# Kernel optimization log

Measured on AMD Instinct MI355X. Metric: run time of the kernel, lower is better.

Reference implementation:

```python
import jax, jax.numpy as jnp
import numpy as np

B, S, D = 4, 4096, 1024

def setup_inputs() -> dict:
    key = jax.random.key(0)
    ks = jax.random.split(key, 11)
    scale = 1.0 / np.sqrt(D)
    def lin(k):
        return jax.random.normal(k, (D, D), dtype=jnp.float32) * scale
    return {
        "x": jax.random.normal(ks[0], (B, S, D), dtype=jnp.float32),
        "Wq": lin(ks[1]), "bq": jax.random.normal(ks[2], (D,), dtype=jnp.float32) * 0.02,
        "Wk": lin(ks[3]), "bk": jax.random.normal(ks[4], (D,), dtype=jnp.float32) * 0.02,
        "Wv": lin(ks[5]), "bv": jax.random.normal(ks[6], (D,), dtype=jnp.float32) * 0.02,
        "W1": lin(ks[7]), "b1": jax.random.normal(ks[8], (D,), dtype=jnp.float32) * 0.02,
        "W2": lin(ks[9]), "b2": jax.random.normal(ks[10], (D,), dtype=jnp.float32) * 0.02,
    }

def reference(x, Wq, bq, Wk, bk, Wv, bv, W1, b1, W2, b2):
    d = x.shape[-1]
    # Single-head self-attention with residual (faithful to source)
    q = x @ Wq + bq  # [B,S,D]
    k = x @ Wk + bk
    v = x @ Wv + bv
    scores = jnp.einsum('bsd,btd->bst', q, k) / jnp.sqrt(jnp.float32(d))  # [B,S,S]
    attn = jax.nn.softmax(scores, axis=-1)
    x = x + jnp.einsum('bst,btd->bsd', attn, v)
    # FeedForward: fc2(relu(fc1(x))), then doubled (x = x + x in source)
    h = jax.nn.relu(x @ W1 + b1)
    y = h @ W2 + b2
    return y + y
```

## Files before the change

### kernel.cpp

```cpp
#include <hip/hip_runtime.h>
#include <stdint.h>

typedef unsigned short u16;
typedef __bf16 bf16x8 __attribute__((ext_vector_type(8)));
typedef float f32x4 __attribute__((ext_vector_type(4)));
typedef unsigned short u16x8 __attribute__((ext_vector_type(8)));
typedef unsigned short u16x4 __attribute__((ext_vector_type(4)));

__device__ __forceinline__ float b2f(u16 b) {
    return __uint_as_float(((unsigned)b) << 16);
}
__device__ __forceinline__ u16 f2b(float f) {
    unsigned u = __float_as_uint(f);
    unsigned r = (u + 0x7fffu + ((u >> 16) & 1u)) >> 16;
    return (u16)r;
}

#define GLDS16(g, l) __builtin_amdgcn_global_load_lds(                        \
    (const __attribute__((address_space(1))) void*)(g),                       \
    (__attribute__((address_space(3))) void*)(l), 16, 0, 0)

template<int HAS_BIAS, int RELU, int HAS_RES, int OUT_MODE>
__device__ __forceinline__ void gemm9_body(
    const u16* __restrict__ A, const u16* __restrict__ Bt,
    const float* __restrict__ bias, const float* __restrict__ res,
    void* __restrict__ Cout, int N, int K,
    long sA, long sB, long sC, long sR, float scale)
{
    __shared__ u16 smem[65536];

    const long nwg = (long)gridDim.x * gridDim.y * gridDim.z;
    long gid = ((long)blockIdx.z * gridDim.y + blockIdx.y) * gridDim.x + blockIdx.x;
    long logical = (nwg % 8 == 0) ? (gid & 7) * (nwg >> 3) + (gid >> 3) : gid;
    const int bx = (int)(logical % gridDim.x);
    long tmp = logical / gridDim.x;
    const int by = (int)(tmp % gridDim.y);
    const int bz = (int)(tmp / gridDim.y);

    A  += (long)bz * sA;
    Bt += (long)bz * sB;

    const int tid  = threadIdx.x;
    const int lane = tid & 63, wid = tid >> 6;
    const int wm   = wid >> 2, wn = wid & 3;
    const int lr   = lane & 15, lk = lane >> 4;
    const long m0  = (long)by * 256;
    const long n0  = (long)bx * 256;
    const int  NT  = K >> 6;

    const u16* gA0 = A  + (m0 + (tid >> 2)) * (long)K + (tid & 3) * 8;
    const u16* gB0 = Bt + (n0 + (tid >> 2)) * (long)K + (tid & 3) * 8;
    const u16* gA1 = gA0 + 128L * K;
    const u16* gB1 = gB0 + 128L * K;
    const int wdst = (tid & ~63) * 8;

#define STA(bufn, kk, kof) do {                                               \
    GLDS16(gA0 + (kof) + (kk) * 32, &smem[(bufn)*16384 + (kk)*8192 + wdst]);  \
    GLDS16(gA1 + (kof) + (kk) * 32, &smem[(bufn)*16384 + (kk)*8192 + wdst + 4096]); } while (0)
#define STB(bufn, kk, kof) do {                                               \
    GLDS16(gB0 + (kof) + (kk) * 32, &smem[32768 + (bufn)*16384 + (kk)*8192 + wdst]); \
    GLDS16(gB1 + (kof) + (kk) * 32, &smem[32768 + (bufn)*16384 + (kk)*8192 + wdst + 4096]); } while (0)

    const int raOff = (wm * 128 + lr) * 32 + lk * 8;
    const int rbOff = (wn * 64  + lr) * 32 + lk * 8;

#define DSA(dst, BUF, kk, ih) do { _Pragma("unroll")                          \
    for (int i = 0; i < 4; ++i)                                               \
        dst[i] = *(const bf16x8*)&smem[(BUF)*16384 + (kk)*8192 + raOff + ((ih)*4 + i)*512]; } while (0)
#define DSB(dst, BUF, kk) do { _Pragma("unroll")                              \
    for (int j = 0; j < 4; ++j)                                               \
        dst[j] = *(const bf16x8*)&smem[32768 + (BUF)*16384 + (kk)*8192 + rbOff + j*512]; } while (0)

#define LGK(n) do { asm volatile("s_waitcnt lgkmcnt(" #n ")" ::: "memory");   \
                    __builtin_amdgcn_sched_barrier(0); } while (0)
#define CKPT(n) do { asm volatile("s_waitcnt vmcnt(" #n ")" ::: "memory");    \
    __builtin_amdgcn_s_barrier(); __builtin_amdgcn_sched_barrier(0); } while (0)

#define MFM(IH, A_, B_) do { __builtin_amdgcn_s_setprio(1); _Pragma("unroll") \
    for (int i = 0; i < 4; ++i) _Pragma("unroll")                             \
        for (int j = 0; j < 4; ++j)                                           \
            acc[(IH)*4 + i][j] = __builtin_amdgcn_mfma_f32_16x16x32_bf16(     \
                A_[i], B_[j], acc[(IH)*4 + i][j], 0, 0, 0);                   \
    __builtin_amdgcn_s_setprio(0); } while (0)

#define TILE_MAIN(BUF, kof) do {                                              \
    DSA(aY, BUF, 0, 1);                 STA((BUF)^1, 0, kof);                 \
    LGK(4);  MFM(0, aX, bX);                                                  \
    CKPT(2);                                                                  \
    DSA(aX, BUF, 1, 0);  DSB(bY, BUF, 1);  STB((BUF)^1, 0, kof);              \
    LGK(8);  MFM(1, aY, bX);                                                  \
    DSA(aY, BUF, 1, 1);                 STA((BUF)^1, 1, kof);                 \
    LGK(4);  MFM(0, aX, bY);                                                  \
    CKPT(2);                                                                  \
    DSA(aX, (BUF)^1, 0, 0);  DSB(bX, (BUF)^1, 0);  STB((BUF)^1, 1, kof);      \
    LGK(8);  MFM(1, aY, bY);                                                  \
} while (0)

#define TILE_LAST(BUF) do {                                                   \
    DSA(aY, BUF, 0, 1);                                                       \
    LGK(4);  MFM(0, aX, bX);                                                  \
    CKPT(0);                                                                  \
    DSA(aX, BUF, 1, 0);  DSB(bY, BUF, 1);                                     \
    LGK(8);  MFM(1, aY, bX);                                                  \
    DSA(aY, BUF, 1, 1);                                                       \
    LGK(4);  MFM(0, aX, bY);                                                  \
    LGK(0);  MFM(1, aY, bY);                                                  \
} while (0)

    f32x4 acc[8][4];
    #pragma unroll
    for (int i = 0; i < 8; ++i)
        #pragma unroll
        for (int j = 0; j < 4; ++j)
            #pragma unroll
            for (int r = 0; r < 4; ++r) acc[i][j][r] = 0.0f;

    bf16x8 aX[4], aY[4], bX[4], bY[4];

    STA(0, 0, 0); STB(0, 0, 0); STA(0, 1, 0); STB(0, 1, 0);
    CKPT(4);
    DSA(aX, 0, 0, 0); DSB(bX, 0, 0);

    #pragma unroll 1
    for (int t = 0; t + 2 < NT; t += 2) {
        TILE_MAIN(0, (long)(t + 1) * 64);
        TILE_MAIN(1, (long)(t + 2) * 64);
    }
    TILE_MAIN(0, (long)(NT - 1) * 64);
    TILE_LAST(1);

    const long crow0 = m0 + wm * 128;
    const long ccol0 = n0 + wn * 64;
    u16*   Cb = (u16*)Cout   + (long)bz * sC;
    float* Cf = (float*)Cout + (long)bz * sC;
    const float* resz = res + (long)bz * sR;
    #pragma unroll
    for (int i = 0; i < 8; ++i) {
        #pragma unroll
        for (int j = 0; j < 4; ++j) {
            const long col = ccol0 + j * 16 + lr;
            float bv_ = 0.0f;
            if (HAS_BIAS) bv_ = bias[col];
            if (OUT_MODE == 2) {
                const long row0 = crow0 + i * 16 + lk * 4;
                u16x4 pk;
                #pragma unroll
                for (int r = 0; r < 4; ++r) {
                    float v = acc[i][j][r] + bv_;
                    v *= scale;
                    pk[r] = f2b(v);
                }
                const long b_ = row0 >> 12, s_ = row0 & 4095;
                *(u16x4*)((u16*)Cout + (b_ << 22) + (col << 12) + s_) = pk;
            } else {
                #pragma unroll
                for (int r = 0; r < 4; ++r) {
                    const long row = crow0 + i * 16 + lk * 4 + r;
                    float v = acc[i][j][r];
                    if (HAS_BIAS) v += bv_;
                    v *= scale;
                    if (RELU) v = fmaxf(v, 0.0f);
                    if (HAS_RES) v += resz[row * (long)N + col];
                    if (OUT_MODE == 1) Cf[row * (long)N + col] = v;
                    else               Cb[row * (long)N + col] = f2b(v);
                }
            }
        }
    }
#undef STA
#undef STB
#undef DSA
#undef DSB
#undef LGK
#undef CKPT
#undef MFM
#undef TILE_MAIN
#undef TILE_LAST
}

__global__ __launch_bounds__(512, 2) void g9_proj(
    const u16* A, const u16* Bt, const float* bias, u16* C, int N, int K)
{ gemm9_body<1,0,0,0>(A, Bt, bias, nullptr, C, N, K, 0,0,0,0, 1.0f); }

__global__ __launch_bounds__(512, 2) void g9_vproj(
    const u16* A, const u16* Bt, const float* bias, u16* C, int N, int K)
{ gemm9_body<1,0,0,2>(A, Bt, bias, nullptr, C, N, K, 0,0,0,0, 1.0f); }

__global__ __launch_bounds__(512, 2) void g9_qkt(
    const u16* A, const u16* Bt, u16* C, int N, int K,
    long sA, long sB, long sC, float scale)
{ gemm9_body<0,0,0,0>(A, Bt, nullptr, nullptr, C, N, K, sA, sB, sC, 0, scale); }

__global__ __launch_bounds__(512, 2) void g9_pv(
    const u16* A, const u16* Bt, const float* res, u16* C, int N, int K,
    long sA, long sB, long sC, long sR)
{ gemm9_body<0,0,1,0>(A, Bt, nullptr, res, C, N, K, sA, sB, sC, sR, 1.0f); }

__global__ __launch_bounds__(512, 2) void g9_ffn1(
    const u16* A, const u16* Bt, const float* bias, u16* C, int N, int K)
{ gemm9_body<1,1,0,0>(A, Bt, bias, nullptr, C, N, K, 0,0,0,0, 1.0f); }

__global__ __launch_bounds__(512, 2) void g9_ffn2(
    const u16* A, const u16* Bt, const float* bias, float* C, int N, int K, float scale)
{ gemm9_body<1,0,0,1>(A, Bt, bias, nullptr, C, N, K, 0,0,0,0, scale); }

__global__ __launch_bounds__(256) void cvt_f32_bf16(
    const float* __restrict__ in, u16* __restrict__ out, long n)
{
    long i = ((long)blockIdx.x * 256 + threadIdx.x) * 4;
    if (i >= n) return;
    float4 f = *(const float4*)(in + i);
    u16x4 o;
    o[0] = f2b(f.x); o[1] = f2b(f.y); o[2] = f2b(f.z); o[3] = f2b(f.w);
    *(u16x4*)(out + i) = o;
}

__global__ __launch_bounds__(256) void transpose_to_bf16(
    const float* __restrict__ in, u16* __restrict__ out, int R, int C)
{
    __shared__ float tile[32][33];
    const int bx = blockIdx.x * 32;
    const int by = blockIdx.y * 32;
    const int tx = threadIdx.x, ty = threadIdx.y;
    #pragma unroll
    for (int i = 0; i < 32; i += 8)
        tile[ty + i][tx] = in[(long)(by + ty + i) * C + bx + tx];
    __syncthreads();
    #pragma unroll
    for (int i = 0; i < 32; i += 8)
        out[(long)(bx + ty + i) * R + by + tx] = f2b(tile[tx][ty + i]);
}

__global__ __launch_bounds__(256) void softmax_rows(u16* __restrict__ P, int n)
{
    const int t = threadIdx.x;
    const int lane = t & 63, w = t >> 6;
    u16* row = P + (long)blockIdx.x * n;
    u16x8 a = *(const u16x8*)(row + t * 16);
    u16x8 b = *(const u16x8*)(row + t * 16 + 8);
    float v[16];
    #pragma unroll
    for (int i = 0; i < 8; ++i) { v[i] = b2f(a[i]); v[8 + i] = b2f(b[i]); }

    float mx = v[0];
    #pragma unroll
    for (int i = 1; i < 16; ++i) mx = fmaxf(mx, v[i]);
    #pragma unroll
    for (int o = 32; o > 0; o >>= 1) mx = fmaxf(mx, __shfl_xor(mx, o));
    __shared__ float red[8];
    if (lane == 0) red[w] = mx;
    __syncthreads();
    mx = fmaxf(fmaxf(red[0], red[1]), fmaxf(red[2], red[3]));

    float s = 0.0f;
    #pragma unroll
    for (int i = 0; i < 16; ++i) { v[i] = __expf(v[i] - mx); s += v[i]; }
    #pragma unroll
    for (int o = 32; o > 0; o >>= 1) s += __shfl_xor(s, o);
    if (lane == 0) red[4 + w] = s;
    __syncthreads();
    s = red[4] + red[5] + red[6] + red[7];
    const float inv = 1.0f / s;

    #pragma unroll
    for (int i = 0; i < 8; ++i) { a[i] = f2b(v[i] * inv); b[i] = f2b(v[8 + i] * inv); }
    *(u16x8*)(row + t * 16)     = a;
    *(u16x8*)(row + t * 16 + 8) = b;
}

extern "C" void kernel_launch(void* const* d_in, const int* in_sizes, int n_in,
                              void* d_out, int out_size, void* d_ws, size_t ws_size,
                              hipStream_t stream)
{
    (void)in_sizes; (void)n_in; (void)out_size;
    const float* x  = (const float*)d_in[0];
    const float* Wq = (const float*)d_in[1];
    const float* bq = (const float*)d_in[2];
    const float* Wk = (const float*)d_in[3];
    const float* bk = (const float*)d_in[4];
    const float* Wv = (const float*)d_in[5];
    const float* bv = (const float*)d_in[6];
    const float* W1 = (const float*)d_in[7];
    const float* b1 = (const float*)d_in[8];
    const float* W2 = (const float*)d_in[9];
    const float* b2 = (const float*)d_in[10];
    float* out = (float*)d_out;

    const int  B = 4, S = 4096, D = 1024;
    const long SD  = (long)S * D;
    const long BSD = (long)B * SD;
    const long SS  = (long)S * S;

    int BC = 4;
    while (BC > 1 && (size_t)((long)BC * SS + 5L * D * D + 3L * BSD) * 2 > ws_size)
        BC >>= 1;

    u16* Pb = (u16*)d_ws;
    u16* xb = Pb;
    u16* Wt = Pb + (long)BC * SS;
    u16* Qb = Wt + 5L * D * D;
    u16* Kb = Qb + BSD;
    u16* Vt = Kb + BSD;

    cvt_f32_bf16<<<dim3((unsigned)(BSD / 4 / 256)), 256, 0, stream>>>(x, xb, BSD);

    dim3 tb(32, 8);
    transpose_to_bf16<<<dim3(D / 32, D / 32), tb, 0, stream>>>(Wq, Wt + 0L * D * D, D, D);
    transpose_to_bf16<<<dim3(D / 32, D / 32), tb, 0, stream>>>(Wk, Wt + 1L * D * D, D, D);
    transpose_to_bf16<<<dim3(D / 32, D / 32), tb, 0, stream>>>(Wv, Wt + 2L * D * D, D, D);
    transpose_to_bf16<<<dim3(D / 32, D / 32), tb, 0, stream>>>(W1, Wt + 3L * D * D, D, D);
    transpose_to_bf16<<<dim3(D / 32, D / 32), tb, 0, stream>>>(W2, Wt + 4L * D * D, D, D);

    const dim3 gproj(D / 256, (B * S) / 256);
    g9_proj <<<gproj, 512, 0, stream>>>(xb, Wt + 0L*D*D, bq, Qb, D, D);
    g9_proj <<<gproj, 512, 0, stream>>>(xb, Wt + 1L*D*D, bk, Kb, D, D);
    g9_vproj<<<gproj, 512, 0, stream>>>(xb, Wt + 2L*D*D, bv, Vt, D, D);

    for (int c = 0; c < B; c += BC) {
        g9_qkt<<<dim3(S/256, S/256, BC), 512, 0, stream>>>(
            Qb + (long)c * SD, Kb + (long)c * SD, Pb, S, D, SD, SD, SS, 0.03125f);
        softmax_rows<<<BC * S, 256, 0, stream>>>(Pb, S);
        g9_pv<<<dim3(D/256, S/256, BC), 512, 0, stream>>>(
            Pb, Vt + (long)c * SD, x + (long)c * SD, Kb + (long)c * SD,
            D, S, SS, SD, SD, SD);
    }

    g9_ffn1<<<gproj, 512, 0, stream>>>(Kb, Wt + 3L*D*D, b1, Qb, D, D);
    g9_ffn2<<<gproj, 512, 0, stream>>>(Qb, Wt + 4L*D*D, b2, out, D, D, 2.0f);
}
```

Measured before the change: 546.2 us.

## Restructure GEMM main loop into full k-slice phases with deeper prefetch

The GEMM inner schedule now loads all 8 A fragments and 4 B fragments per k-slice and issues 32 MFMAs per phase, replacing the four half-tile phases. Global-to-LDS prefetch runs one extra half-tile ahead, with three stages in flight at the prologue and a separate penultimate tile step. The aim is fewer barriers and waitcnt points per tile and more latency hiding for the LDS loads. In exchange, A-fragment register usage doubles, which may pressure the 2-waves-per-SIMD occupancy target, and LDS buffer reuse becomes tighter.

```diff
diff --git a/kernel.cpp b/kernel.cpp
--- a/kernel.cpp
+++ b/kernel.cpp
@@ -21,7 +21,7 @@
     (__attribute__((address_space(3))) void*)(l), 16, 0, 0)
 
 template<int HAS_BIAS, int RELU, int HAS_RES, int OUT_MODE>
-__device__ __forceinline__ void gemm9_body(
+__device__ __forceinline__ void gemm10_body(
     const u16* __restrict__ A, const u16* __restrict__ Bt,
     const float* __restrict__ bias, const float* __restrict__ res,
     void* __restrict__ Cout, int N, int K,
@@ -64,10 +64,10 @@
     const int raOff = (wm * 128 + lr) * 32 + lk * 8;
     const int rbOff = (wn * 64  + lr) * 32 + lk * 8;
 
-#define DSA(dst, BUF, kk, ih) do { _Pragma("unroll")                          \
-    for (int i = 0; i < 4; ++i)                                               \
-        dst[i] = *(const bf16x8*)&smem[(BUF)*16384 + (kk)*8192 + raOff + ((ih)*4 + i)*512]; } while (0)
-#define DSB(dst, BUF, kk) do { _Pragma("unroll")                              \
+#define DSA8(dst, BUF, kk) do { _Pragma("unroll")                             \
+    for (int i = 0; i < 8; ++i)                                               \
+        dst[i] = *(const bf16x8*)&smem[(BUF)*16384 + (kk)*8192 + raOff + i*512]; } while (0)
+#define DSB4(dst, BUF, kk) do { _Pragma("unroll")                             \
     for (int j = 0; j < 4; ++j)                                               \
         dst[j] = *(const bf16x8*)&smem[32768 + (BUF)*16384 + (kk)*8192 + rbOff + j*512]; } while (0)
 
@@ -76,35 +76,34 @@
 #define CKPT(n) do { asm volatile("s_waitcnt vmcnt(" #n ")" ::: "memory");    \
     __builtin_amdgcn_s_barrier(); __builtin_amdgcn_sched_barrier(0); } while (0)
 
-#define MFM(IH, A_, B_) do { __builtin_amdgcn_s_setprio(1); _Pragma("unroll") \
-    for (int i = 0; i < 4; ++i) _Pragma("unroll")                             \
+#define MFM32(A_, B_) do { __builtin_amdgcn_s_setprio(1); _Pragma("unroll")   \
+    for (int i = 0; i < 8; ++i) _Pragma("unroll")                             \
         for (int j = 0; j < 4; ++j)                                           \
-            acc[(IH)*4 + i][j] = __builtin_amdgcn_mfma_f32_16x16x32_bf16(     \
-                A_[i], B_[j], acc[(IH)*4 + i][j], 0, 0, 0);                   \
+            acc[i][j] = __builtin_amdgcn_mfma_f32_16x16x32_bf16(              \
+                A_[i], B_[j], acc[i][j], 0, 0, 0);                            \
     __builtin_amdgcn_s_setprio(0); } while (0)
 
-#define TILE_MAIN(BUF, kof) do {                                              \
-    DSA(aY, BUF, 0, 1);                 STA((BUF)^1, 0, kof);                 \
-    LGK(4);  MFM(0, aX, bX);                                                  \
-    CKPT(2);                                                                  \
-    DSA(aX, BUF, 1, 0);  DSB(bY, BUF, 1);  STB((BUF)^1, 0, kof);              \
-    LGK(8);  MFM(1, aY, bX);                                                  \
-    DSA(aY, BUF, 1, 1);                 STA((BUF)^1, 1, kof);                 \
-    LGK(4);  MFM(0, aX, bY);                                                  \
-    CKPT(2);                                                                  \
-    DSA(aX, (BUF)^1, 0, 0);  DSB(bX, (BUF)^1, 0);  STB((BUF)^1, 1, kof);      \
-    LGK(8);  MFM(1, aY, bY);                                                  \
+#define TILE_FULL(BUF, kof1, kof2) do {                                       \
+    DSA8(aY, BUF, 1);  DSB4(bY, BUF, 1);                                      \
+    STA((BUF)^1, 1, kof1);  STB((BUF)^1, 1, kof1);                            \
+    LGK(12);  MFM32(aX, bX);  CKPT(4);                                        \
+    DSA8(aX, (BUF)^1, 0);  DSB4(bX, (BUF)^1, 0);                              \
+    STA(BUF, 0, kof2);  STB(BUF, 0, kof2);                                    \
+    LGK(12);  MFM32(aY, bY);  CKPT(4);                                        \
 } while (0)
 
+#define TILE_PEN(BUF, kof1) do {                                              \
+    DSA8(aY, BUF, 1);  DSB4(bY, BUF, 1);                                      \
+    STA((BUF)^1, 1, kof1);  STB((BUF)^1, 1, kof1);                            \
+    LGK(12);  MFM32(aX, bX);  CKPT(4);                                        \
+    DSA8(aX, (BUF)^1, 0);  DSB4(bX, (BUF)^1, 0);                              \
+    LGK(12);  MFM32(aY, bY);  CKPT(0);                                        \
+} while (0)
+
 #define TILE_LAST(BUF) do {                                                   \
-    DSA(aY, BUF, 0, 1);                                                       \
-    LGK(4);  MFM(0, aX, bX);                                                  \
-    CKPT(0);                                                                  \
-    DSA(aX, BUF, 1, 0);  DSB(bY, BUF, 1);                                     \
-    LGK(8);  MFM(1, aY, bX);                                                  \
-    DSA(aY, BUF, 1, 1);                                                       \
-    LGK(4);  MFM(0, aX, bY);                                                  \
-    LGK(0);  MFM(1, aY, bY);                                                  \
+    DSA8(aY, BUF, 1);  DSB4(bY, BUF, 1);                                      \
+    LGK(12);  MFM32(aX, bX);                                                  \
+    LGK(0);   MFM32(aY, bY);                                                  \
 } while (0)
 
     f32x4 acc[8][4];
@@ -115,18 +114,21 @@
             #pragma unroll
             for (int r = 0; r < 4; ++r) acc[i][j][r] = 0.0f;
 
-    bf16x8 aX[4], aY[4], bX[4], bY[4];
-
-    STA(0, 0, 0); STB(0, 0, 0); STA(0, 1, 0); STB(0, 1, 0);
+    bf16x8 aX[8], aY[8], bX[4], bY[4];
+
+    STA(0, 0, 0); STB(0, 0, 0);
+    STA(0, 1, 0); STB(0, 1, 0);
+    STA(1, 0, 64); STB(1, 0, 64);
+    CKPT(8);
+    DSA8(aX, 0, 0); DSB4(bX, 0, 0);
     CKPT(4);
-    DSA(aX, 0, 0, 0); DSB(bX, 0, 0);
 
     #pragma unroll 1
-    for (int t = 0; t + 2 < NT; t += 2) {
-        TILE_MAIN(0, (long)(t + 1) * 64);
-        TILE_MAIN(1, (long)(t + 2) * 64);
+    for (int t = 0; t + 3 < NT; t += 2) {
+        TILE_FULL(0, (long)(t + 1) * 64, (long)(t + 2) * 64);
+        TILE_FULL(1, (long)(t + 2) * 64, (long)(t + 3) * 64);
     }
-    TILE_MAIN(0, (long)(NT - 1) * 64);
+    TILE_PEN(0, (long)(NT - 1) * 64);
     TILE_LAST(1);
 
     const long crow0 = m0 + wm * 128;
@@ -169,40 +171,41 @@
     }
 #undef STA
 #undef STB
-#undef DSA
-#undef DSB
+#undef DSA8
+#undef DSB4
 #undef LGK
 #undef CKPT
-#undef MFM
-#undef TILE_MAIN
+#undef MFM32
+#undef TILE_FULL
+#undef TILE_PEN
 #undef TILE_LAST
 }
 
-__global__ __launch_bounds__(512, 2) void g9_proj(
+__global__ __launch_bounds__(512, 2) void g10_proj(
     const u16* A, const u16* Bt, const float* bias, u16* C, int N, int K)
-{ gemm9_body<1,0,0,0>(A, Bt, bias, nullptr, C, N, K, 0,0,0,0, 1.0f); }
-
-__global__ __launch_bounds__(512, 2) void g9_vproj(
+{ gemm10_body<1,0,0,0>(A, Bt, bias, nullptr, C, N, K, 0,0,0,0, 1.0f); }
+
+__global__ __launch_bounds__(512, 2) void g10_vproj(
     const u16* A, const u16* Bt, const float* bias, u16* C, int N, int K)
-{ gemm9_body<1,0,0,2>(A, Bt, bias, nullptr, C, N, K, 0,0,0,0, 1.0f); }
-
-__global__ __launch_bounds__(512, 2) void g9_qkt(
+{ gemm10_body<1,0,0,2>(A, Bt, bias, nullptr, C, N, K, 0,0,0,0, 1.0f); }
+
+__global__ __launch_bounds__(512, 2) void g10_qkt(
     const u16* A, const u16* Bt, u16* C, int N, int K,
     long sA, long sB, long sC, float scale)
-{ gemm9_body<0,0,0,0>(A, Bt, nullptr, nullptr, C, N, K, sA, sB, sC, 0, scale); }
-
-__global__ __launch_bounds__(512, 2) void g9_pv(
+{ gemm10_body<0,0,0,0>(A, Bt, nullptr, nullptr, C, N, K, sA, sB, sC, 0, scale); }
+
+__global__ __launch_bounds__(512, 2) void g10_pv(
     const u16* A, const u16* Bt, const float* res, u16* C, int N, int K,
     long sA, long sB, long sC, long sR)
-{ gemm9_body<0,0,1,0>(A, Bt, nullptr, res, C, N, K, sA, sB, sC, sR, 1.0f); }
-
-__global__ __launch_bounds__(512, 2) void g9_ffn1(
+{ gemm10_body<0,0,1,0>(A, Bt, nullptr, res, C, N, K, sA, sB, sC, sR, 1.0f); }
+
+__global__ __launch_bounds__(512, 2) void g10_ffn1(
     const u16* A, const u16* Bt, const float* bias, u16* C, int N, int K)
-{ gemm9_body<1,1,0,0>(A, Bt, bias, nullptr, C, N, K, 0,0,0,0, 1.0f); }
-
-__global__ __launch_bounds__(512, 2) void g9_ffn2(
+{ gemm10_body<1,1,0,0>(A, Bt, bias, nullptr, C, N, K, 0,0,0,0, 1.0f); }
+
+__global__ __launch_bounds__(512, 2) void g10_ffn2(
     const u16* A, const u16* Bt, const float* bias, float* C, int N, int K, float scale)
-{ gemm9_body<1,0,0,1>(A, Bt, bias, nullptr, C, N, K, 0,0,0,0, scale); }
+{ gemm10_body<1,0,0,1>(A, Bt, bias, nullptr, C, N, K, 0,0,0,0, scale); }
 
 __global__ __launch_bounds__(256) void cvt_f32_bf16(
     const float* __restrict__ in, u16* __restrict__ out, long n)
@@ -312,19 +315,19 @@
     transpose_to_bf16<<<dim3(D / 32, D / 32), tb, 0, stream>>>(W2, Wt + 4L * D * D, D, D);
 
     const dim3 gproj(D / 256, (B * S) / 256);
-    g9_proj <<<gproj, 512, 0, stream>>>(xb, Wt + 0L*D*D, bq, Qb, D, D);
-    g9_proj <<<gproj, 512, 0, stream>>>(xb, Wt + 1L*D*D, bk, Kb, D, D);
-    g9_vproj<<<gproj, 512, 0, stream>>>(xb, Wt + 2L*D*D, bv, Vt, D, D);
+    g10_proj <<<gproj, 512, 0, stream>>>(xb, Wt + 0L*D*D, bq, Qb, D, D);
+    g10_proj <<<gproj, 512, 0, stream>>>(xb, Wt + 1L*D*D, bk, Kb, D, D);
+    g10_vproj<<<gproj, 512, 0, stream>>>(xb, Wt + 2L*D*D, bv, Vt, D, D);
 
     for (int c = 0; c < B; c += BC) {
-        g9_qkt<<<dim3(S/256, S/256, BC), 512, 0, stream>>>(
+        g10_qkt<<<dim3(S/256, S/256, BC), 512, 0, stream>>>(
             Qb + (long)c * SD, Kb + (long)c * SD, Pb, S, D, SD, SD, SS, 0.03125f);
         softmax_rows<<<BC * S, 256, 0, stream>>>(Pb, S);
-        g9_pv<<<dim3(D/256, S/256, BC), 512, 0, stream>>>(
+        g10_pv<<<dim3(D/256, S/256, BC), 512, 0, stream>>>(
             Pb, Vt + (long)c * SD, x + (long)c * SD, Kb + (long)c * SD,
             D, S, SS, SD, SD, SD);
     }
 
-    g9_ffn1<<<gproj, 512, 0, stream>>>(Kb, Wt + 3L*D*D, b1, Qb, D, D);
-    g9_ffn2<<<gproj, 512, 0, stream>>>(Qb, Wt + 4L*D*D, b2, out, D, D, 2.0f);
-}
+    g10_ffn1<<<gproj, 512, 0, stream>>>(Kb, Wt + 3L*D*D, b1, Qb, D, D);
+    g10_ffn2<<<gproj, 512, 0, stream>>>(Qb, Wt + 4L*D*D, b2, out, D, D, 2.0f);
+}
```

Result: slower. 589.6 us (+7.9%).
